# Kernel optimization log

Measured on AMD Instinct MI355X. Metric: run time of the kernel, lower is better.

Reference implementation:

```python
import jax, jax.numpy as jnp
import numpy as np

N = 20000      # nodes
E = 160000     # edges
F_IN = 64      # node_feature_dim
HID = 256      # hidden_dim (= per-head out_channels, concat=False)
HEADS = 4
OUT = 2
BN_EPS = 1e-5


def setup_inputs() -> dict:
    key = jax.random.key(0)
    ks = jax.random.split(key, 24)
    s = 0.02

    def w(k, shape):
        return jax.random.normal(k, shape, jnp.float32) * s

    return {
        "node_feature": jax.random.normal(ks[0], (N, F_IN), jnp.float32),
        "edge_index": jax.random.randint(ks[1], (2, E), 0, N, jnp.int32),
        # layer 1 (in=F_IN)
        "wq1": w(ks[2], (F_IN, HEADS * HID)), "bq1": w(ks[3], (HEADS * HID,)),
        "wk1": w(ks[4], (F_IN, HEADS * HID)), "bk1": w(ks[5], (HEADS * HID,)),
        "wv1": w(ks[6], (F_IN, HEADS * HID)), "bv1": w(ks[7], (HEADS * HID,)),
        "ws1": w(ks[8], (F_IN, HID)),        "bs1": w(ks[9], (HID,)),
        # layer 2 (in=HID)
        "wq2": w(ks[10], (HID, HEADS * HID)), "bq2": w(ks[11], (HEADS * HID,)),
        "wk2": w(ks[12], (HID, HEADS * HID)), "bk2": w(ks[13], (HEADS * HID,)),
        "wv2": w(ks[14], (HID, HEADS * HID)), "bv2": w(ks[15], (HEADS * HID,)),
        "ws2": w(ks[16], (HID, HID)),         "bs2": w(ks[17], (HID,)),
        # batch norm affine
        "bn_gamma": jnp.ones((HID,), jnp.float32) + w(ks[18], (HID,)),
        "bn_beta": w(ks[19], (HID,)),
        # final linear
        "lin_w": w(ks[20], (HID, OUT)), "lin_b": w(ks[21], (OUT,)),
    }


def _transformer_conv(x, src, dst, wq, bq, wk, bk, wv, bv, ws, bs):
    """PyG TransformerConv, heads=HEADS, concat=False (mean over heads), root_weight."""
    n = x.shape[0]
    q = (x @ wq + bq).reshape(n, HEADS, HID)   # [N,H,C]
    k = (x @ wk + bk).reshape(n, HEADS, HID)
    v = (x @ wv + bv).reshape(n, HEADS, HID)
    # per-edge attention logits: q_i . k_j / sqrt(C)   (message j->i, i = dst)
    alpha = jnp.einsum('ehc,ehc->eh', q[dst], k[src]) / jnp.sqrt(jnp.float32(HID))  # [E,H]
    # scatter-softmax over incoming edges of each target node
    m = jax.ops.segment_max(alpha, dst, num_segments=n)
    m = jnp.where(jnp.isfinite(m), m, 0.0)  # nodes with no in-edges
    ex = jnp.exp(alpha - m[dst])
    denom = jax.ops.segment_sum(ex, dst, num_segments=n)
    a = ex / (denom[dst] + 1e-16)                          # [E,H]
    out = jax.ops.segment_sum(v[src] * a[..., None], dst, num_segments=n)  # [N,H,C]
    return out.mean(axis=1) + x @ ws + bs                  # concat=False -> head mean; + skip


def reference(node_feature, edge_index,
              wq1, bq1, wk1, bk1, wv1, bv1, ws1, bs1,
              wq2, bq2, wk2, bk2, wv2, bv2, ws2, bs2,
              bn_gamma, bn_beta, lin_w, lin_b):
    src, dst = edge_index[0], edge_index[1]
    x = _transformer_conv(node_feature, src, dst, wq1, bq1, wk1, bk1, wv1, bv1, ws1, bs1)
    x = _transformer_conv(x, src, dst, wq2, bq2, wk2, bk2, wv2, bv2, ws2, bs2)
    # BatchNorm1d (training mode: batch statistics, biased variance)
    mu = x.mean(axis=0)
    var = jnp.mean(jnp.square(x - mu), axis=0)
    x = bn_gamma * (x - mu) / jnp.sqrt(var + BN_EPS) + bn_beta
    rsu_embedding = x[0:1]                     # [1, HID]
    logits = jax.nn.relu(x @ lin_w + lin_b)    # [N, OUT]
    action_prob = jax.nn.softmax(logits, axis=1)
    return (action_prob, rsu_embedding)
```

## Files before the change

kernel.cpp:

```cpp
#include <hip/hip_runtime.h>
#include <hip/hip_bf16.h>
#include <math.h>

#define DI __device__ __forceinline__

constexpr int NN   = 20000;
constexpr int NE   = 160000;
constexpr int FIN  = 64;
constexpr int HIDC = 256;

typedef __attribute__((ext_vector_type(8))) short short8;
typedef __attribute__((ext_vector_type(4))) float f32x4;

DI float bf2f(unsigned short u) { return __uint_as_float(((unsigned)u) << 16); }

DI void gld16(const void* g, void* l) {
  __builtin_amdgcn_global_load_lds((const __attribute__((address_space(1))) unsigned*)g,
                                   (__attribute__((address_space(3))) unsigned*)l, 16, 0, 0);
}

__global__ void k_prep(const float* __restrict__ x, __hip_bfloat16* __restrict__ xb,
                       const int* __restrict__ dst, int* __restrict__ deg) {
  int gid = blockIdx.x * 256 + threadIdx.x;
  if (gid < NN * FIN) xb[gid] = __float2bfloat16(x[gid]);
  if (gid < NE) atomicAdd(&deg[dst[gid]], 1);
}

__global__ void k_scan(const int* __restrict__ deg, int* __restrict__ offs,
                       int* __restrict__ cursor, int n_) {
  __shared__ int part[1024];
  int tid = threadIdx.x;
  const int CH = (n_ + 1023) >> 10;
  int base = tid * CH;
  int s = 0;
  for (int i = 0; i < CH; ++i) { int idx = base + i; if (idx < n_) s += deg[idx]; }
  part[tid] = s;
  __syncthreads();
  for (int off = 1; off < 1024; off <<= 1) {
    int v = (tid >= off) ? part[tid - off] : 0;
    __syncthreads();
    part[tid] += v;
    __syncthreads();
  }
  int run = (tid == 0) ? 0 : part[tid - 1];
  for (int i = 0; i < CH; ++i) {
    int idx = base + i;
    if (idx < n_) { offs[idx] = run; cursor[idx] = run; run += deg[idx]; }
  }
  if (tid == 1023) offs[n_] = run;
}

__global__ void k_scatter(const int* __restrict__ dst, int* __restrict__ cursor,
                          int* __restrict__ eid, int e_) {
  int e = blockIdx.x * blockDim.x + threadIdx.x;
  if (e < e_) {
    int p = atomicAdd(&cursor[dst[e]], 1);
    eid[p] = e;
  }
}

__global__ void k_sortsse(const int* __restrict__ offs, int* __restrict__ eid,
                          const int* __restrict__ src, int* __restrict__ sse, int n_) {
  int n = blockIdx.x * 256 + threadIdx.x;
  if (n >= n_) return;
  int s0 = offs[n], s1 = offs[n + 1];
  for (int i = s0 + 1; i < s1; ++i) {
    int v = eid[i];
    int j = i - 1;
    while (j >= s0 && eid[j] > v) { eid[j + 1] = eid[j]; --j; }
    eid[j + 1] = v;
  }
  for (int i = s0; i < s1; ++i) sse[i] = src[eid[i]];
}

__global__ void k_tr(const float* __restrict__ wq, const float* __restrict__ wk,
                     float* __restrict__ WqT, float* __restrict__ WkT, int IN_) {
  int gid = blockIdx.x * 256 + threadIdx.x;
  if (gid >= 1024 * IN_) return;
  int k = gid % IN_, j = gid / IN_;
  WqT[gid] = wq[(size_t)k * 1024 + j];
  WkT[gid] = wk[(size_t)k * 1024 + j];
}

template <int IN>
__global__ void k_mfill(const float* __restrict__ WqT, const float* __restrict__ WkT,
                        const float* __restrict__ bq, const float* __restrict__ bk,
                        const float* __restrict__ ws, const float* __restrict__ bs,
                        __hip_bfloat16* __restrict__ Wt, float* __restrict__ biasp) {
  constexpr int YW = 4 * IN;
  constexpr int CPB = 256 / IN;
  int k = threadIdx.x % IN;
  int sub = threadIdx.x / IN;
  int c = blockIdx.x * CPB + sub;
  float val = 0.f, bval = 0.f;
  if (c < YW) {
    int h = c / IN, i = c % IN;
    const float* wqp = WqT + (size_t)(h * 256) * IN + k;
    const float* wkp = WkT + (size_t)(h * 256) * IN + i;
    float s = 0.f;
#pragma unroll 4
    for (int j = 0; j < 256; ++j) s = fmaf(wqp[(size_t)j * IN], wkp[(size_t)j * IN], s);
    val = s;
  } else if (c < YW + 256) {
    int sc = c - YW;
    val = ws[(size_t)k * 256 + sc];
    bval = bs[sc];
  } else if (c < YW + 260) {
    int h = c - (YW + 256);
    const float* wqp = WqT + (size_t)(h * 256) * IN + k;
    const float* bkp = bk + h * 256;
    float s = 0.f;
#pragma unroll 4
    for (int j = 0; j < 256; ++j) s = fmaf(wqp[(size_t)j * IN], bkp[j], s);
    val = s;
    if (k == 0) {
      float bb = 0.f;
      for (int j = 0; j < 256; ++j) bb = fmaf(bq[h * 256 + j], bk[h * 256 + j], bb);
      bval = bb;
    }
  } else if (c < YW + 264) {
    int h = c - (YW + 260);
    const float* wkp = WkT + (size_t)(h * 256) * IN + k;
    const float* bqp = bq + h * 256;
    float s = 0.f;
#pragma unroll 4
    for (int j = 0; j < 256; ++j) s = fmaf(wkp[(size_t)j * IN], bqp[j], s);
    val = s;
  }
  Wt[(size_t)c * IN + k] = __float2bfloat16(val);
  if (k == 0) biasp[c] = bval;
}

template <int IN>
__global__ void k_pack2(const float* __restrict__ wv, const float* __restrict__ bv,
                        __hip_bfloat16* __restrict__ Wt2, float* __restrict__ bias2) {
  constexpr int K2 = 4 * IN;
  int gid = blockIdx.x * 256 + threadIdx.x;
  int col = gid / K2, k = gid % K2;
  int h = k / IN, d = k % IN;
  Wt2[gid] = __float2bfloat16(0.25f * wv[(size_t)d * 1024 + h * 256 + col]);
  if (k == 0)
    bias2[col] = 0.25f * (bv[col] + bv[256 + col] + bv[512 + col] + bv[768 + col]);
}

template <int IN>
__global__ __launch_bounds__(64, 2) void k_gemm1(
    const __hip_bfloat16* __restrict__ X, const __hip_bfloat16* __restrict__ Wt,
    const float* __restrict__ biasp,
    __hip_bfloat16* __restrict__ Ybuf, float* __restrict__ skipf,
    float* __restrict__ CDbuf, int nrows, int NCB, int NCH, int TPC, int RT) {
  __shared__ char lds[16384 + 2304];
  const int l = threadIdx.x;
  constexpr int K = IN;
  constexpr int YW = 4 * IN;
  const int nwg = NCB * NCH;
  const int per = nwg >> 3;
  const int w = (blockIdx.x & 7) * per + (blockIdx.x >> 3);
  const int chunk = w / NCB;
  const int ct = w % NCB;
  const int bn = ct * 64;
  const int t0 = chunk * TPC;
  int t1 = t0 + TPC; if (t1 > RT) t1 = RT;
  constexpr int KT = K / 64;
  constexpr int NS = K / 32;

  const int lm = l & 15, lk = l >> 4;

  short8 bfr[4 * NS];
  {
    const __hip_bfloat16* bp = Wt + (size_t)(bn + lm) * K + lk * 8;
#pragma unroll
    for (int n = 0; n < 4; ++n)
#pragma unroll
      for (int s = 0; s < NS; ++s)
        bfr[n * NS + s] = *(const short8*)(bp + (size_t)n * 16 * K + s * 32);
  }
  float bia[4];
#pragma unroll
  for (int n = 0; n < 4; ++n) bia[n] = biasp[bn + n * 16 + lm];

  const int mode = (bn < YW) ? 0 : ((bn < YW + 256) ? 1 : 2);

  const int jrow = l >> 3;
  const int cslot = (l & 7) ^ jrow;
  auto STAGE = [&](int buf, int t, int kt) {
    char* db = lds + buf * 8192;
#pragma unroll
    for (int j = 0; j < 8; ++j) {
      int r = t * 64 + j * 8 + jrow;
      if (r >= nrows) r = nrows - 1;
      gld16(X + (size_t)r * K + kt * 64 + cslot * 8, db + j * 1024 + l * 16);
    }
  };

  int buf = 0;
  STAGE(0, t0, 0);
  for (int t = t0; t < t1; ++t) {
    f32x4 acc[4][4] = {};
#pragma unroll
    for (int kt = 0; kt < KT; ++kt) {
      int nt = t, nk = kt + 1;
      if (nk == KT) { nt = (t + 1 < t1) ? t + 1 : t; nk = 0; }
      STAGE(buf ^ 1, nt, nk);
      asm volatile("s_waitcnt vmcnt(8)" ::: "memory");
      const char* db = lds + buf * 8192;
#pragma unroll
      for (int s2 = 0; s2 < 2; ++s2) {
        short8 a[4];
#pragma unroll
        for (int m = 0; m < 4; ++m) {
          int row = m * 16 + lm;
          a[m] = *(const short8*)(db + row * 128 + (((s2 * 4 + lk) ^ (lm & 7)) * 16));
        }
#pragma unroll
        for (int m = 0; m < 4; ++m)
#pragma unroll
          for (int n = 0; n < 4; ++n)
            acc[m][n] = __builtin_amdgcn_mfma_f32_16x16x32_bf16(
                a[m], bfr[n * NS + kt * 2 + s2], acc[m][n], 0, 0, 0);
      }
      buf ^= 1;
    }

    const int tbase = t * 64;
    if (mode == 0) {
      char* sc = lds + 16384;
      const int srow = l >> 2, qc = l & 3;
#pragma unroll
      for (int m = 0; m < 4; ++m) {
#pragma unroll
        for (int n = 0; n < 4; ++n)
#pragma unroll
          for (int r = 0; r < 4; ++r)
            *(__hip_bfloat16*)(sc + (lk * 4 + r) * 144 + (n * 16 + lm) * 2) =
                __float2bfloat16(acc[m][n][r] + bia[n]);
        const char* sr = sc + srow * 144 + qc * 32;
        short8 ta = *(const short8*)(sr);
        short8 tb = *(const short8*)(sr + 16);
        int grow = tbase + m * 16 + srow;
        if (grow < nrows) {
          ushort* o = (ushort*)Ybuf + (size_t)grow * YW + bn + qc * 16;
          *(short8*)o = ta;
          *(short8*)(o + 8) = tb;
        }
      }
    } else if (mode == 1) {
      const int cb = bn - YW;
#pragma unroll
      for (int m = 0; m < 4; ++m)
#pragma unroll
        for (int n = 0; n < 4; ++n)
#pragma unroll
          for (int r = 0; r < 4; ++r) {
            int row = tbase + m * 16 + lk * 4 + r;
            if (row < nrows) skipf[(size_t)row * HIDC + cb + n * 16 + lm] = acc[m][n][r] + bia[n];
          }
    } else {
#pragma unroll
      for (int m = 0; m < 4; ++m)
#pragma unroll
        for (int n = 0; n < 4; ++n) {
          int cl = n * 16 + lm;
          if (cl < 8) {
#pragma unroll
            for (int r = 0; r < 4; ++r) {
              int row = tbase + m * 16 + lk * 4 + r;
              if (row < nrows) CDbuf[(size_t)row * 8 + cl] = acc[m][n][r] + bia[n];
            }
          }
        }
    }
  }
  asm volatile("s_waitcnt vmcnt(0)" ::: "memory");
}

template <int IN>
__global__ __launch_bounds__(256) void k_attn(
    const __hip_bfloat16* __restrict__ Ybuf, const __hip_bfloat16* __restrict__ Xs,
    const float* __restrict__ CD, const int* __restrict__ offs,
    const int* __restrict__ sse, __hip_bfloat16* __restrict__ Zbuf,
    float* __restrict__ Abuf) {
  constexpr int DPL = IN / 16;
  constexpr int YW = 4 * IN;
  int n = blockIdx.x * 4 + (threadIdx.x >> 6);
  if (n >= NN) return;
  int lane = threadIdx.x & 63;
  int h = lane >> 4, j = lane & 15;
  int s0 = offs[n];
  int deg = offs[n + 1] - s0;
  ushort* zr = (ushort*)Zbuf + (size_t)n * YW + h * IN + j * DPL;
  if (deg == 0) {
#pragma unroll
    for (int d = 0; d < DPL; ++d) zr[d] = 0;
    if (lane == 0) Abuf[n] = 0.f;
    return;
  }

  float y[DPL];
  {
    const ushort* yr = (const ushort*)Ybuf + (size_t)n * YW + h * IN + j * DPL;
    if constexpr (IN == 256) {
      short8 y0 = *(const short8*)yr;
      short8 y1 = *(const short8*)(yr + 8);
#pragma unroll
      for (int d = 0; d < 8; ++d) {
        y[d] = bf2f((unsigned short)y0[d]);
        y[8 + d] = bf2f((unsigned short)y1[d]);
      }
    } else {
      short4 yv = *(const short4*)yr;
      y[0] = bf2f((unsigned short)yv.x);
      y[1] = bf2f((unsigned short)yv.y);
      y[2] = bf2f((unsigned short)yv.z);
      y[3] = bf2f((unsigned short)yv.w);
    }
  }
  float C = CD[(size_t)n * 8 + h];
  float acc[DPL] = {};
  float denom = 0.f;
  const int* se = sse + s0;
  const ushort* xb = (const ushort*)Xs;

#define LOADE(P, E)                                                     \
  {                                                                     \
    int e_ = (E);                                                       \
    int s_ = se[(e_ < deg) ? e_ : 0];                                   \
    const ushort* xp_ = xb + (size_t)s_ * IN + j * DPL;                 \
    if constexpr (IN == 256) {                                          \
      P##0 = *(const short8*)xp_;                                       \
      P##1 = *(const short8*)(xp_ + 8);                                 \
    } else {                                                            \
      P##s = *(const short4*)xp_;                                       \
    }                                                                   \
    P##D = CD[(size_t)s_ * 8 + 4 + h];                                  \
  }

#define COMPE(P, E)                                                     \
  {                                                                     \
    float xf[DPL];                                                      \
    if constexpr (IN == 256) {                                          \
      _Pragma("unroll") for (int d = 0; d < 8; ++d) {                   \
        xf[d] = bf2f((unsigned short)P##0[d]);                          \
        xf[8 + d] = bf2f((unsigned short)P##1[d]);                      \
      }                                                                 \
    } else {                                                            \
      xf[0] = bf2f((unsigned short)P##s.x);                             \
      xf[1] = bf2f((unsigned short)P##s.y);                             \
      xf[2] = bf2f((unsigned short)P##s.z);                             \
      xf[3] = bf2f((unsigned short)P##s.w);                             \
    }                                                                   \
    float p_ = 0.f;                                                     \
    _Pragma("unroll") for (int d = 0; d < DPL; ++d) p_ = fmaf(y[d], xf[d], p_); \
    p_ += __shfl_xor(p_, 1);                                            \
    p_ += __shfl_xor(p_, 2);                                            \
    p_ += __shfl_xor(p_, 4);                                            \
    p_ += __shfl_xor(p_, 8);                                            \
    float w_ = ((E) < deg) ? __expf((p_ + C + P##D) * 0.0625f) : 0.f;   \
    denom += w_;                                                        \
    _Pragma("unroll") for (int d = 0; d < DPL; ++d) acc[d] = fmaf(w_, xf[d], acc[d]); \
  }

  short8 A0, A1, B0, B1;
  short4 As, Bs;
  float AD, BD;
  (void)As; (void)Bs; (void)A0; (void)A1; (void)B0; (void)B1;
  LOADE(A, 0);
  for (int e = 0; e < deg; e += 2) {
    LOADE(B, e + 1);
    COMPE(A, e);
    LOADE(A, e + 2);
    COMPE(B, e + 1);
  }
#undef LOADE
#undef COMPE

  float dinv = 1.f / (denom + 1e-16f);
  if constexpr (IN == 256) {
    short8 o0, o1;
#pragma unroll
    for (int d = 0; d < 8; ++d) {
      o0[d] = (short)__bfloat16_as_ushort(__float2bfloat16(acc[d] * dinv));
      o1[d] = (short)__bfloat16_as_ushort(__float2bfloat16(acc[8 + d] * dinv));
    }
    *(short8*)zr = o0;
    *(short8*)(zr + 8) = o1;
  } else {
    short4 o;
    o.x = (short)__bfloat16_as_ushort(__float2bfloat16(acc[0] * dinv));
    o.y = (short)__bfloat16_as_ushort(__float2bfloat16(acc[1] * dinv));
    o.z = (short)__bfloat16_as_ushort(__float2bfloat16(acc[2] * dinv));
    o.w = (short)__bfloat16_as_ushort(__float2bfloat16(acc[3] * dinv));
    *(short4*)zr = o;
  }
  if (lane == 0) Abuf[n] = 1.f;
}

template <int K2, bool F32OUT>
__global__ __launch_bounds__(64, 3) void k_gemm2(
    const __hip_bfloat16* __restrict__ Z, const __hip_bfloat16* __restrict__ Wt2,
    const float* __restrict__ bias2, const float* __restrict__ Abuf,
    const float* __restrict__ skipf, void* __restrict__ outp, int nrows) {
  __shared__ char lds[8192];
  const int l = threadIdx.x;
  int bid = blockIdx.x;
  {
    int nwg = gridDim.x;
    int q8 = nwg >> 3, r8 = nwg & 7;
    int xcd = bid & 7, idx = bid >> 3;
    bid = (xcd < r8 ? xcd * (q8 + 1) : r8 * (q8 + 1) + (xcd - r8) * q8) + idx;
  }
  const int tile = bid >> 2;
  const int bn = (bid & 3) * 64;
  constexpr int KT = K2 / 64;
  const int lm = l & 15, lk = l >> 4;
  const int jrow = l >> 3, cslot = (l & 7) ^ jrow;

  float bia[4];
#pragma unroll
  for (int n = 0; n < 4; ++n) bia[n] = bias2[bn + n * 16 + lm];

  const __hip_bfloat16* bp = Wt2 + (size_t)(bn + lm) * K2 + lk * 8;

  auto ISSUE_A = [&](int buf, int ch) {
    char* db = lds + buf * 4096;
#pragma unroll
    for (int jj = 0; jj < 4; ++jj) {
      int r = tile * 32 + jj * 8 + jrow;
      if (r >= nrows) r = nrows - 1;
      gld16(Z + (size_t)r * K2 + ch * 64 + cslot * 8, db + jj * 1024 + l * 16);
    }
  };

  short8 bA[4][2], bB[4][2];
#define ISSUE_B(DST, CH)                                                    \
  {                                                                         \
    int ch_ = (CH);                                                         \
    _Pragma("unroll") for (int n = 0; n < 4; ++n)                           \
      _Pragma("unroll") for (int s2 = 0; s2 < 2; ++s2)                      \
        DST[n][s2] = *(const short8*)(bp + (size_t)n * 16 * K2 + ch_ * 64 + s2 * 32); \
  }

  f32x4 acc[2][4] = {};
#define COMPUTE(BSRC, BUF)                                                  \
  {                                                                         \
    const char* db = lds + (BUF) * 4096;                                    \
    _Pragma("unroll") for (int s2 = 0; s2 < 2; ++s2) {                      \
      short8 a[2];                                                          \
      _Pragma("unroll") for (int m = 0; m < 2; ++m) {                       \
        int row = m * 16 + lm;                                              \
        a[m] = *(const short8*)(db + row * 128 + (((s2 * 4 + lk) ^ (lm & 7)) * 16)); \
      }                                                                     \
      _Pragma("unroll") for (int m = 0; m < 2; ++m)                         \
        _Pragma("unroll") for (int n = 0; n < 4; ++n)                       \
          acc[m][n] = __builtin_amdgcn_mfma_f32_16x16x32_bf16(a[m], BSRC[n][s2], acc[m][n], 0, 0, 0); \
    }                                                                       \
  }

  ISSUE_B(bA, 0);
  ISSUE_A(0, 0);
  for (int ch = 0; ch < KT; ch += 2) {
    int c1 = ch + 1;
    ISSUE_B(bB, c1);
    ISSUE_A(1, c1);
    asm volatile("s_waitcnt vmcnt(12)" ::: "memory");
    COMPUTE(bA, 0);
    int c2 = (ch + 2 < KT) ? ch + 2 : c1;
    ISSUE_B(bA, c2);
    ISSUE_A(0, c2);
    asm volatile("s_waitcnt vmcnt(12)" ::: "memory");
    COMPUTE(bB, 1);
  }
#undef ISSUE_B
#undef COMPUTE

  const int tbase = tile * 32;
#pragma unroll
  for (int m = 0; m < 2; ++m)
#pragma unroll
    for (int r = 0; r < 4; ++r) {
      int row = tbase + m * 16 + lk * 4 + r;
      if (row >= nrows) continue;
      float af = Abuf[row];
#pragma unroll
      for (int n = 0; n < 4; ++n) {
        int col = bn + n * 16 + lm;
        float v = acc[m][n][r] + af * bia[n] + skipf[(size_t)row * HIDC + col];
        if constexpr (F32OUT)
          ((float*)outp)[(size_t)row * HIDC + col] = v;
        else
          ((ushort*)outp)[(size_t)row * HIDC + col] = __bfloat16_as_ushort(__float2bfloat16(v));
      }
    }
  asm volatile("s_waitcnt vmcnt(0)" ::: "memory");
}

__global__ void k_bnstats(const float* __restrict__ x, float* __restrict__ psum,
                          float* __restrict__ psumsq) {
  int t = threadIdx.x, b = blockIdx.x;
  float s = 0.f, s2 = 0.f;
  for (int r = b; r < NN; r += 256) {
    float vv = x[(size_t)r * HIDC + t];
    s += vv; s2 += vv * vv;
  }
  psum[b * HIDC + t] = s;
  psumsq[b * HIDC + t] = s2;
}

__global__ void k_bnred(const float* __restrict__ psum, const float* __restrict__ psumsq,
                        float* __restrict__ sums, float* __restrict__ sumsq) {
  int t = threadIdx.x;
  float s = 0.f, s2 = 0.f;
  for (int b = 0; b < 256; ++b) { s += psum[b * HIDC + t]; s2 += psumsq[b * HIDC + t]; }
  sums[t] = s;
  sumsq[t] = s2;
}

__global__ __launch_bounds__(256) void k_final(
    const float* __restrict__ x, const float* __restrict__ sums, const float* __restrict__ sumsq,
    const float* __restrict__ gamma, const float* __restrict__ beta,
    const float* __restrict__ lw, const float* __restrict__ lb,
    float* __restrict__ out, int n_) {
  int sub = threadIdx.x >> 6, lane = threadIdx.x & 63;
  int n = blockIdx.x * 4 + sub;
  if (n >= n_) return;
  int c = lane * 4;
  float4 sm  = *(const float4*)(sums + c);
  float4 sq  = *(const float4*)(sumsq + c);
  const float inv_n = 1.f / (float)n_;
  float mu0 = sm.x * inv_n, mu1 = sm.y * inv_n, mu2 = sm.z * inv_n, mu3 = sm.w * inv_n;
  float r0 = 1.f / sqrtf(fmaxf(sq.x * inv_n - mu0 * mu0, 0.f) + 1e-5f);
  float r1 = 1.f / sqrtf(fmaxf(sq.y * inv_n - mu1 * mu1, 0.f) + 1e-5f);
  float r2 = 1.f / sqrtf(fmaxf(sq.z * inv_n - mu2 * mu2, 0.f) + 1e-5f);
  float r3 = 1.f / sqrtf(fmaxf(sq.w * inv_n - mu3 * mu3, 0.f) + 1e-5f);
  const float* xr = x + (size_t)n * HIDC;
  float4 xv = *(const float4*)(xr + c);
  float4 gv = *(const float4*)(gamma + c);
  float4 bv = *(const float4*)(beta + c);
  float y0 = gv.x * (xv.x - mu0) * r0 + bv.x;
  float y1 = gv.y * (xv.y - mu1) * r1 + bv.y;
  float y2 = gv.z * (xv.z - mu2) * r2 + bv.z;
  float y3 = gv.w * (xv.w - mu3) * r3 + bv.w;
  float4 wa = *(const float4*)(lw + (size_t)c * 2);
  float4 wb = *(const float4*)(lw + (size_t)c * 2 + 4);
  float p0 = y0 * wa.x + y1 * wa.z + y2 * wb.x + y3 * wb.z;
  float p1 = y0 * wa.y + y1 * wa.w + y2 * wb.y + y3 * wb.w;
#pragma unroll
  for (int off = 32; off > 0; off >>= 1) {
    p0 += __shfl_xor(p0, off);
    p1 += __shfl_xor(p1, off);
  }
  if (n == 0) *(float4*)(out + (size_t)NN * 2 + c) = make_float4(y0, y1, y2, y3);
  if (lane == 0) {
    float l0 = fmaxf(p0 + lb[0], 0.f);
    float l1 = fmaxf(p1 + lb[1], 0.f);
    float m = fmaxf(l0, l1);
    float e0 = expf(l0 - m), e1 = expf(l1 - m);
    float inv = 1.f / (e0 + e1);
    out[(size_t)n * 2 + 0] = e0 * inv;
    out[(size_t)n * 2 + 1] = e1 * inv;
  }
}

extern "C" void kernel_launch(void* const* d_in, const int* in_sizes, int n_in,
                              void* d_out, int out_size, void* d_ws, size_t ws_size,
                              hipStream_t stream) {
  const float* x0  = (const float*)d_in[0];
  const int*   ei  = (const int*)d_in[1];
  const float* wq1 = (const float*)d_in[2];  const float* bq1 = (const float*)d_in[3];
  const float* wk1 = (const float*)d_in[4];  const float* bk1 = (const float*)d_in[5];
  const float* wv1 = (const float*)d_in[6];  const float* bv1 = (const float*)d_in[7];
  const float* ws1 = (const float*)d_in[8];  const float* bs1 = (const float*)d_in[9];
  const float* wq2 = (const float*)d_in[10]; const float* bq2 = (const float*)d_in[11];
  const float* wk2 = (const float*)d_in[12]; const float* bk2 = (const float*)d_in[13];
  const float* wv2 = (const float*)d_in[14]; const float* bv2 = (const float*)d_in[15];
  const float* ws2 = (const float*)d_in[16]; const float* bs2 = (const float*)d_in[17];
  const float* gam = (const float*)d_in[18]; const float* bet = (const float*)d_in[19];
  const float* lw  = (const float*)d_in[20]; const float* lb  = (const float*)d_in[21];
  const int* srcv = ei;
  const int* dstv = ei + NE;

  char* p = (char*)d_ws;
  auto take = [&](size_t bytes) {
    char* r = p;
    p += (bytes + 255) & ~(size_t)255;
    return r;
  };
  __hip_bfloat16* Ybuf = (__hip_bfloat16*)take((size_t)NN * 1024 * 2);
  __hip_bfloat16* Zbuf = (__hip_bfloat16*)take((size_t)NN * 1024 * 2);
  float* skipf = (float*)take((size_t)NN * HIDC * 4);
  float* x3    = (float*)take((size_t)NN * HIDC * 4);
  __hip_bfloat16* x0b = (__hip_bfloat16*)take((size_t)NN * FIN * 2);
  __hip_bfloat16* x2b = (__hip_bfloat16*)take((size_t)NN * HIDC * 2);
  float* CDbuf = (float*)take((size_t)NN * 8 * 4);
  float* Abuf  = (float*)take((size_t)NN * 4);
  __hip_bfloat16* Wt1a = (__hip_bfloat16*)take((size_t)576 * 64 * 2);
  __hip_bfloat16* Wt1b = (__hip_bfloat16*)take((size_t)1344 * 256 * 2);
  float* bias1a = (float*)take(576 * 4);
  float* bias1b = (float*)take(1344 * 4);
  __hip_bfloat16* Wt2a = (__hip_bfloat16*)take((size_t)256 * 256 * 2);
  __hip_bfloat16* Wt2b = (__hip_bfloat16*)take((size_t)256 * 1024 * 2);
  float* bias2a = (float*)take(256 * 4);
  float* bias2b = (float*)take(256 * 4);
  float* WqTa = (float*)take((size_t)1024 * 64 * 4);
  float* WkTa = (float*)take((size_t)1024 * 64 * 4);
  float* WqTb = (float*)take((size_t)1024 * 256 * 4);
  float* WkTb = (float*)take((size_t)1024 * 256 * 4);
  float* psum  = (float*)take(256 * HIDC * 4);
  float* psumsq= (float*)take(256 * HIDC * 4);
  float* bnbuf = (float*)take(2 * HIDC * 4);
  int* deg    = (int*)take((size_t)NN * 4);
  int* offs   = (int*)take((size_t)(NN + 1) * 4);
  int* cursor = (int*)take((size_t)NN * 4);
  int* eidb   = (int*)take((size_t)NE * 4);
  int* sse    = (int*)take((size_t)NE * 4);
  if ((size_t)(p - (char*)d_ws) > ws_size) return;

  float* sums  = bnbuf;
  float* sumsq = bnbuf + HIDC;

  hipMemsetAsync(deg, 0, (size_t)NN * 4, stream);
  k_prep<<<(NN * FIN + 255) / 256, 256, 0, stream>>>(x0, x0b, dstv, deg);
  k_scan<<<1, 1024, 0, stream>>>(deg, offs, cursor, NN);
  k_scatter<<<(NE + 255) / 256, 256, 0, stream>>>(dstv, cursor, eidb, NE);
  k_sortsse<<<(NN + 255) / 256, 256, 0, stream>>>(offs, eidb, srcv, sse, NN);

  k_tr<<<(1024 * 64 + 255) / 256, 256, 0, stream>>>(wq1, wk1, WqTa, WkTa, 64);
  k_mfill<64><<<144, 256, 0, stream>>>(WqTa, WkTa, bq1, bk1, ws1, bs1, Wt1a, bias1a);
  k_pack2<64><<<256, 256, 0, stream>>>(wv1, bv1, Wt2a, bias2a);
  k_tr<<<(1024 * 256 + 255) / 256, 256, 0, stream>>>(wq2, wk2, WqTb, WkTb, 256);
  k_mfill<256><<<1344, 256, 0, stream>>>(WqTb, WkTb, bq2, bk2, ws2, bs2, Wt1b, bias1b);
  k_pack2<256><<<1024, 256, 0, stream>>>(wv2, bv2, Wt2b, bias2b);

  const int RT  = (NN + 63) / 64;
  const int NCH = 40;
  const int TPC = (RT + NCH - 1) / NCH;
  const int AG = (NN + 3) / 4;
  const int NRT32 = (NN + 31) / 32;
  const int G2 = NRT32 * 4;

  k_gemm1<64><<<9 * NCH, 64, 0, stream>>>(x0b, Wt1a, bias1a, Ybuf, skipf, CDbuf, NN, 9, NCH, TPC, RT);
  k_attn<64><<<AG, 256, 0, stream>>>(Ybuf, x0b, CDbuf, offs, sse, Zbuf, Abuf);
  k_gemm2<256, false><<<G2, 64, 0, stream>>>(Zbuf, Wt2a, bias2a, Abuf, skipf, x2b, NN);
  k_gemm1<256><<<21 * NCH, 64, 0, stream>>>(x2b, Wt1b, bias1b, Ybuf, skipf, CDbuf, NN, 21, NCH, TPC, RT);
  k_attn<256><<<AG, 256, 0, stream>>>(Ybuf, x2b, CDbuf, offs, sse, Zbuf, Abuf);
  k_gemm2<1024, true><<<G2, 64, 0, stream>>>(Zbuf, Wt2b, bias2b, Abuf, skipf, x3, NN);
  k_bnstats<<<256, 256, 0, stream>>>(x3, psum, psumsq);
  k_bnred<<<1, 256, 0, stream>>>(psum, psumsq, sums, sumsq);
  k_final<<<(NN + 3) / 4, 256, 0, stream>>>(x3, sums, sumsq, gam, bet, lw, lb, (float*)d_out, NN);
}
```

Before: 382.3 us.

## Fuse edge attention aggregation with output projection GEMM via LDS staging

Merges the attention aggregation kernel and the following V-projection GEMM into one kernel. Each 512-thread block aggregates 32 nodes into a swizzled LDS tile, then applies MFMA against the packed weights and adds bias and skip. This removes the Zbuf and Abuf global round trips and one launch per layer. In exchange, each block reloads the full weight slice from global memory, and a large LDS tile (64KB for the second layer) limits occupancy. The grid also relies on NN being divisible by 32.

```diff
diff --git a/kernel.cpp b/kernel.cpp
--- a/kernel.cpp
+++ b/kernel.cpp
@@ -274,52 +274,66 @@
   asm volatile("s_waitcnt vmcnt(0)" ::: "memory");
 }
 
-template <int IN>
-__global__ __launch_bounds__(256) void k_attn(
+template <int IN, bool F32OUT>
+__global__ __launch_bounds__(512) void k_attn_out(
     const __hip_bfloat16* __restrict__ Ybuf, const __hip_bfloat16* __restrict__ Xs,
     const float* __restrict__ CD, const int* __restrict__ offs,
-    const int* __restrict__ sse, __hip_bfloat16* __restrict__ Zbuf,
-    float* __restrict__ Abuf) {
+    const int* __restrict__ sse, const __hip_bfloat16* __restrict__ Wt2,
+    const float* __restrict__ bias2, const float* __restrict__ skipf,
+    void* __restrict__ outp) {
+  constexpr int K2 = 4 * IN;
   constexpr int DPL = IN / 16;
   constexpr int YW = 4 * IN;
-  int n = blockIdx.x * 4 + (threadIdx.x >> 6);
-  if (n >= NN) return;
-  int lane = threadIdx.x & 63;
-  int h = lane >> 4, j = lane & 15;
-  int s0 = offs[n];
-  int deg = offs[n + 1] - s0;
-  ushort* zr = (ushort*)Zbuf + (size_t)n * YW + h * IN + j * DPL;
-  if (deg == 0) {
-#pragma unroll
-    for (int d = 0; d < DPL; ++d) zr[d] = 0;
-    if (lane == 0) Abuf[n] = 0.f;
-    return;
-  }
-
-  float y[DPL];
-  {
-    const ushort* yr = (const ushort*)Ybuf + (size_t)n * YW + h * IN + j * DPL;
-    if constexpr (IN == 256) {
-      short8 y0 = *(const short8*)yr;
-      short8 y1 = *(const short8*)(yr + 8);
-#pragma unroll
-      for (int d = 0; d < 8; ++d) {
-        y[d] = bf2f((unsigned short)y0[d]);
-        y[8 + d] = bf2f((unsigned short)y1[d]);
+  __shared__ __align__(16) char Zs[32 * K2 * 2];
+  const int w = threadIdx.x >> 6, lane = threadIdx.x & 63;
+  const int h4 = lane >> 4, j = lane & 15;
+  const int nbase = blockIdx.x * 32;
+
+  for (int u = 0; u < 4; ++u) {
+    const int zrow = w * 4 + u;
+    const int n = nbase + zrow;
+    char* zp = Zs + zrow * (K2 * 2);
+    const int sw = (zrow & 7) << 4;
+    const int s0 = offs[n];
+    const int deg = offs[n + 1] - s0;
+    const int cb = (h4 * IN + j * DPL) * 2;
+
+    if (deg == 0) {
+      if constexpr (IN == 256) {
+        short8 z8 = {};
+        *(short8*)(zp + (cb ^ sw)) = z8;
+        *(short8*)(zp + ((cb + 16) ^ sw)) = z8;
+      } else {
+        short4 z4 = {(short)0, (short)0, (short)0, (short)0};
+        *(short4*)(zp + (cb ^ sw)) = z4;
       }
-    } else {
-      short4 yv = *(const short4*)yr;
-      y[0] = bf2f((unsigned short)yv.x);
-      y[1] = bf2f((unsigned short)yv.y);
-      y[2] = bf2f((unsigned short)yv.z);
-      y[3] = bf2f((unsigned short)yv.w);
-    }
-  }
-  float C = CD[(size_t)n * 8 + h];
-  float acc[DPL] = {};
-  float denom = 0.f;
-  const int* se = sse + s0;
-  const ushort* xb = (const ushort*)Xs;
+      continue;
+    }
+
+    float y[DPL];
+    {
+      const ushort* yr = (const ushort*)Ybuf + (size_t)n * YW + h4 * IN + j * DPL;
+      if constexpr (IN == 256) {
+        short8 y0 = *(const short8*)yr;
+        short8 y1 = *(const short8*)(yr + 8);
+#pragma unroll
+        for (int d = 0; d < 8; ++d) {
+          y[d] = bf2f((unsigned short)y0[d]);
+          y[8 + d] = bf2f((unsigned short)y1[d]);
+        }
+      } else {
+        short4 yv = *(const short4*)yr;
+        y[0] = bf2f((unsigned short)yv.x);
+        y[1] = bf2f((unsigned short)yv.y);
+        y[2] = bf2f((unsigned short)yv.z);
+        y[3] = bf2f((unsigned short)yv.w);
+      }
+    }
+    float C = CD[(size_t)n * 8 + h4];
+    float acc[DPL] = {};
+    float denom = 0.f;
+    const int* se = sse + s0;
+    const ushort* xb = (const ushort*)Xs;
 
 #define LOADE(P, E)                                                     \
   {                                                                     \
@@ -332,7 +346,7 @@
     } else {                                                            \
       P##s = *(const short4*)xp_;                                       \
     }                                                                   \
-    P##D = CD[(size_t)s_ * 8 + 4 + h];                                  \
+    P##D = CD[(size_t)s_ * 8 + 4 + h4];                                 \
   }
 
 #define COMPE(P, E)                                                     \
@@ -360,138 +374,103 @@
     _Pragma("unroll") for (int d = 0; d < DPL; ++d) acc[d] = fmaf(w_, xf[d], acc[d]); \
   }
 
-  short8 A0, A1, B0, B1;
-  short4 As, Bs;
-  float AD, BD;
-  (void)As; (void)Bs; (void)A0; (void)A1; (void)B0; (void)B1;
-  LOADE(A, 0);
-  for (int e = 0; e < deg; e += 2) {
-    LOADE(B, e + 1);
-    COMPE(A, e);
-    LOADE(A, e + 2);
-    COMPE(B, e + 1);
-  }
+    short8 A0, A1, B0, B1;
+    short4 As, Bs;
+    float AD, BD;
+    (void)As; (void)Bs; (void)A0; (void)A1; (void)B0; (void)B1;
+    LOADE(A, 0);
+    for (int e = 0; e < deg; e += 2) {
+      LOADE(B, e + 1);
+      COMPE(A, e);
+      LOADE(A, e + 2);
+      COMPE(B, e + 1);
+    }
 #undef LOADE
 #undef COMPE
 
-  float dinv = 1.f / (denom + 1e-16f);
-  if constexpr (IN == 256) {
-    short8 o0, o1;
-#pragma unroll
-    for (int d = 0; d < 8; ++d) {
-      o0[d] = (short)__bfloat16_as_ushort(__float2bfloat16(acc[d] * dinv));
-      o1[d] = (short)__bfloat16_as_ushort(__float2bfloat16(acc[8 + d] * dinv));
-    }
-    *(short8*)zr = o0;
-    *(short8*)(zr + 8) = o1;
-  } else {
-    short4 o;
-    o.x = (short)__bfloat16_as_ushort(__float2bfloat16(acc[0] * dinv));
-    o.y = (short)__bfloat16_as_ushort(__float2bfloat16(acc[1] * dinv));
-    o.z = (short)__bfloat16_as_ushort(__float2bfloat16(acc[2] * dinv));
-    o.w = (short)__bfloat16_as_ushort(__float2bfloat16(acc[3] * dinv));
-    *(short4*)zr = o;
-  }
-  if (lane == 0) Abuf[n] = 1.f;
-}
-
-template <int K2, bool F32OUT>
-__global__ __launch_bounds__(64, 3) void k_gemm2(
-    const __hip_bfloat16* __restrict__ Z, const __hip_bfloat16* __restrict__ Wt2,
-    const float* __restrict__ bias2, const float* __restrict__ Abuf,
-    const float* __restrict__ skipf, void* __restrict__ outp, int nrows) {
-  __shared__ char lds[8192];
-  const int l = threadIdx.x;
-  int bid = blockIdx.x;
-  {
-    int nwg = gridDim.x;
-    int q8 = nwg >> 3, r8 = nwg & 7;
-    int xcd = bid & 7, idx = bid >> 3;
-    bid = (xcd < r8 ? xcd * (q8 + 1) : r8 * (q8 + 1) + (xcd - r8) * q8) + idx;
-  }
-  const int tile = bid >> 2;
-  const int bn = (bid & 3) * 64;
+    float dinv = 1.f / (denom + 1e-16f);
+    if constexpr (IN == 256) {
+      short8 o0, o1;
+#pragma unroll
+      for (int d = 0; d < 8; ++d) {
+        o0[d] = (short)__bfloat16_as_ushort(__float2bfloat16(acc[d] * dinv));
+        o1[d] = (short)__bfloat16_as_ushort(__float2bfloat16(acc[8 + d] * dinv));
+      }
+      *(short8*)(zp + (cb ^ sw)) = o0;
+      *(short8*)(zp + ((cb + 16) ^ sw)) = o1;
+    } else {
+      short4 o;
+      o.x = (short)__bfloat16_as_ushort(__float2bfloat16(acc[0] * dinv));
+      o.y = (short)__bfloat16_as_ushort(__float2bfloat16(acc[1] * dinv));
+      o.z = (short)__bfloat16_as_ushort(__float2bfloat16(acc[2] * dinv));
+      o.w = (short)__bfloat16_as_ushort(__float2bfloat16(acc[3] * dinv));
+      *(short4*)(zp + (cb ^ sw)) = o;
+    }
+  }
+  __syncthreads();
+
+  const int bn = w * 32;
+  const int lm = lane & 15, lk = lane >> 4;
   constexpr int KT = K2 / 64;
-  const int lm = l & 15, lk = l >> 4;
-  const int jrow = l >> 3, cslot = (l & 7) ^ jrow;
-
-  float bia[4];
-#pragma unroll
-  for (int n = 0; n < 4; ++n) bia[n] = bias2[bn + n * 16 + lm];
-
+  float bia[2];
+#pragma unroll
+  for (int n = 0; n < 2; ++n) bia[n] = bias2[bn + n * 16 + lm];
   const __hip_bfloat16* bp = Wt2 + (size_t)(bn + lm) * K2 + lk * 8;
 
-  auto ISSUE_A = [&](int buf, int ch) {
-    char* db = lds + buf * 4096;
-#pragma unroll
-    for (int jj = 0; jj < 4; ++jj) {
-      int r = tile * 32 + jj * 8 + jrow;
-      if (r >= nrows) r = nrows - 1;
-      gld16(Z + (size_t)r * K2 + ch * 64 + cslot * 8, db + jj * 1024 + l * 16);
-    }
-  };
-
-  short8 bA[4][2], bB[4][2];
-#define ISSUE_B(DST, CH)                                                    \
+  short8 bA[2][2], bB[2][2];
+  f32x4 acc2[2][2] = {};
+
+#define LOADB(D, CH)                                                        \
   {                                                                         \
     int ch_ = (CH);                                                         \
-    _Pragma("unroll") for (int n = 0; n < 4; ++n)                           \
+    _Pragma("unroll") for (int n = 0; n < 2; ++n)                           \
       _Pragma("unroll") for (int s2 = 0; s2 < 2; ++s2)                      \
-        DST[n][s2] = *(const short8*)(bp + (size_t)n * 16 * K2 + ch_ * 64 + s2 * 32); \
-  }
-
-  f32x4 acc[2][4] = {};
-#define COMPUTE(BSRC, BUF)                                                  \
+        D[n][s2] = *(const short8*)(bp + (size_t)n * 16 * K2 + ch_ * 64 + s2 * 32); \
+  }
+
+#define COMPB(B, CH)                                                        \
   {                                                                         \
-    const char* db = lds + (BUF) * 4096;                                    \
+    int ch_ = (CH);                                                         \
     _Pragma("unroll") for (int s2 = 0; s2 < 2; ++s2) {                      \
       short8 a[2];                                                          \
       _Pragma("unroll") for (int m = 0; m < 2; ++m) {                       \
         int row = m * 16 + lm;                                              \
-        a[m] = *(const short8*)(db + row * 128 + (((s2 * 4 + lk) ^ (lm & 7)) * 16)); \
+        a[m] = *(const short8*)(Zs + row * (K2 * 2) +                       \
+                ((ch_ * 128 + s2 * 64 + lk * 16) ^ ((row & 7) << 4)));      \
       }                                                                     \
       _Pragma("unroll") for (int m = 0; m < 2; ++m)                         \
-        _Pragma("unroll") for (int n = 0; n < 4; ++n)                       \
-          acc[m][n] = __builtin_amdgcn_mfma_f32_16x16x32_bf16(a[m], BSRC[n][s2], acc[m][n], 0, 0, 0); \
+        _Pragma("unroll") for (int n = 0; n < 2; ++n)                       \
+          acc2[m][n] = __builtin_amdgcn_mfma_f32_16x16x32_bf16(a[m], B[n][s2], acc2[m][n], 0, 0, 0); \
     }                                                                       \
   }
 
-  ISSUE_B(bA, 0);
-  ISSUE_A(0, 0);
+  LOADB(bA, 0);
   for (int ch = 0; ch < KT; ch += 2) {
-    int c1 = ch + 1;
-    ISSUE_B(bB, c1);
-    ISSUE_A(1, c1);
-    asm volatile("s_waitcnt vmcnt(12)" ::: "memory");
-    COMPUTE(bA, 0);
-    int c2 = (ch + 2 < KT) ? ch + 2 : c1;
-    ISSUE_B(bA, c2);
-    ISSUE_A(0, c2);
-    asm volatile("s_waitcnt vmcnt(12)" ::: "memory");
-    COMPUTE(bB, 1);
-  }
-#undef ISSUE_B
-#undef COMPUTE
-
-  const int tbase = tile * 32;
+    LOADB(bB, ch + 1);
+    COMPB(bA, ch);
+    if (ch + 2 < KT) LOADB(bA, ch + 2);
+    COMPB(bB, ch + 1);
+  }
+#undef LOADB
+#undef COMPB
+
 #pragma unroll
   for (int m = 0; m < 2; ++m)
 #pragma unroll
     for (int r = 0; r < 4; ++r) {
-      int row = tbase + m * 16 + lk * 4 + r;
-      if (row >= nrows) continue;
-      float af = Abuf[row];
-#pragma unroll
-      for (int n = 0; n < 4; ++n) {
+      int lr = m * 16 + lk * 4 + r;
+      int g = nbase + lr;
+      float af = (offs[g + 1] > offs[g]) ? 1.f : 0.f;
+#pragma unroll
+      for (int n = 0; n < 2; ++n) {
         int col = bn + n * 16 + lm;
-        float v = acc[m][n][r] + af * bia[n] + skipf[(size_t)row * HIDC + col];
+        float v = acc2[m][n][r] + af * bia[n] + skipf[(size_t)g * HIDC + col];
         if constexpr (F32OUT)
-          ((float*)outp)[(size_t)row * HIDC + col] = v;
+          ((float*)outp)[(size_t)g * HIDC + col] = v;
         else
-          ((ushort*)outp)[(size_t)row * HIDC + col] = __bfloat16_as_ushort(__float2bfloat16(v));
+          ((ushort*)outp)[(size_t)g * HIDC + col] = __bfloat16_as_ushort(__float2bfloat16(v));
       }
     }
-  asm volatile("s_waitcnt vmcnt(0)" ::: "memory");
 }
 
 __global__ void k_bnstats(const float* __restrict__ x, float* __restrict__ psum,
@@ -586,13 +565,11 @@
     return r;
   };
   __hip_bfloat16* Ybuf = (__hip_bfloat16*)take((size_t)NN * 1024 * 2);
-  __hip_bfloat16* Zbuf = (__hip_bfloat16*)take((size_t)NN * 1024 * 2);
   float* skipf = (float*)take((size_t)NN * HIDC * 4);
   float* x3    = (float*)take((size_t)NN * HIDC * 4);
   __hip_bfloat16* x0b = (__hip_bfloat16*)take((size_t)NN * FIN * 2);
   __hip_bfloat16* x2b = (__hip_bfloat16*)take((size_t)NN * HIDC * 2);
   float* CDbuf = (float*)take((size_t)NN * 8 * 4);
-  float* Abuf  = (float*)take((size_t)NN * 4);
   __hip_bfloat16* Wt1a = (__hip_bfloat16*)take((size_t)576 * 64 * 2);
   __hip_bfloat16* Wt1b = (__hip_bfloat16*)take((size_t)1344 * 256 * 2);
   float* bias1a = (float*)take(576 * 4);
@@ -634,16 +611,12 @@
   const int RT  = (NN + 63) / 64;
   const int NCH = 40;
   const int TPC = (RT + NCH - 1) / NCH;
-  const int AG = (NN + 3) / 4;
-  const int NRT32 = (NN + 31) / 32;
-  const int G2 = NRT32 * 4;
+  const int AG = NN / 32;
 
   k_gemm1<64><<<9 * NCH, 64, 0, stream>>>(x0b, Wt1a, bias1a, Ybuf, skipf, CDbuf, NN, 9, NCH, TPC, RT);
-  k_attn<64><<<AG, 256, 0, stream>>>(Ybuf, x0b, CDbuf, offs, sse, Zbuf, Abuf);
-  k_gemm2<256, false><<<G2, 64, 0, stream>>>(Zbuf, Wt2a, bias2a, Abuf, skipf, x2b, NN);
+  k_attn_out<64, false><<<AG, 512, 0, stream>>>(Ybuf, x0b, CDbuf, offs, sse, Wt2a, bias2a, skipf, x2b);
   k_gemm1<256><<<21 * NCH, 64, 0, stream>>>(x2b, Wt1b, bias1b, Ybuf, skipf, CDbuf, NN, 21, NCH, TPC, RT);
-  k_attn<256><<<AG, 256, 0, stream>>>(Ybuf, x2b, CDbuf, offs, sse, Zbuf, Abuf);
-  k_gemm2<1024, true><<<G2, 64, 0, stream>>>(Zbuf, Wt2b, bias2b, Abuf, skipf, x3, NN);
+  k_attn_out<256, true><<<AG, 512, 0, stream>>>(Ybuf, x2b, CDbuf, offs, sse, Wt2b, bias2b, skipf, x3);
   k_bnstats<<<256, 256, 0, stream>>>(x3, psum, psumsq);
   k_bnred<<<1, 256, 0, stream>>>(psum, psumsq, sums, sumsq);
   k_final<<<(NN + 3) / 4, 256, 0, stream>>>(x3, sums, sumsq, gam, bet, lw, lb, (float*)d_out, NN);
```

Measured after the change: 389.3 us. About the same (+1.8%).
